# Kernel optimization log

Hardware: AMD Instinct MI355X
Metric: run time of the kernel (lower is better)

Reference implementation:

```python
import jax, jax.numpy as jnp
import numpy as np

N = 100000
E = 1280000
D = 64


def setup_inputs() -> dict:
    key = jax.random.key(0)
    k1, k2, k3, k4, k5, k6 = jax.random.split(key, 6)
    return {
        "x": jax.random.normal(k1, (N, D), dtype=jnp.float32),
        "w_src": jax.random.normal(k2, (D,), dtype=jnp.float32),
        "w_dst": jax.random.normal(k3, (D,), dtype=jnp.float32),
        "ew": jax.random.normal(k4, (E,), dtype=jnp.float32),
        "src_idx": jax.random.randint(k5, (E,), 0, N, dtype=jnp.int64),
        "dst_idx": jax.random.randint(k6, (E,), 0, N, dtype=jnp.int64),
    }


def reference(x, w_src, w_dst, ew, src_idx, dst_idx):
    # Per-node scalar scores: Linear(emb_dim, 1, bias=False)
    a_src = x @ w_src            # [N]
    a_dst = x @ w_dst            # [N]
    # Edge attention: tanh(a_src[u] + a_dst[v]) * ew  (u_add_v + tanh + scale)
    a = jnp.tanh(a_src[src_idx] + a_dst[dst_idx]) * ew   # [E]
    # Message = a_e * x[src_e]; reduce = scatter-sum over dst (u_mul_e + sum)
    m = a[:, None] * x[src_idx]                           # [E, D]
    h = jax.ops.segment_sum(m, dst_idx, num_segments=N)   # [N, D]
    return h
```

## Files before the change

kernel.cpp:

```cpp
#include <hip/hip_runtime.h>
#include <hip/hip_fp16.h>
#include <math.h>

typedef unsigned long long ull;

#define DIM  64
#define SPAN 256
#define SPAN_SHIFT 8
#define NBIN 256
#define KMAX 512
#define CAP  6144

__global__ __launch_bounds__(256) void score_hist_kernel(
        const float* __restrict__ x,
        const float* __restrict__ w_src,
        const float* __restrict__ w_dst,
        const int* __restrict__ dst_idx,
        float* __restrict__ a_src,
        float* __restrict__ a_dst,
        __half* __restrict__ xh,
        int* __restrict__ cnt,
        int N, int E, int K) {
    __shared__ int lh[KMAX];
    int tid = threadIdx.x;
    int b   = blockIdx.x;
    bool histblk = (b < NBIN);
    if (histblk) {
        for (int j = tid; j < K; j += 256) lh[j] = 0;
        __syncthreads();
    }
    int lane = tid & 63;
    int wave = tid >> 6;
    int grp  = lane >> 4;
    int sub  = lane & 15;
    int node = b * 16 + wave * 4 + grp;
    if (node < N) {
        float4 v  = ((const float4*)x)[(size_t)node * 16 + sub];
        float4 ws = ((const float4*)w_src)[sub];
        float4 wd = ((const float4*)w_dst)[sub];
        float s1 = v.x * ws.x + v.y * ws.y + v.z * ws.z + v.w * ws.w;
        float s2 = v.x * wd.x + v.y * wd.y + v.z * wd.z + v.w * wd.w;
        #pragma unroll
        for (int off = 1; off < 16; off <<= 1) {
            s1 += __shfl_xor(s1, off, 64);
            s2 += __shfl_xor(s2, off, 64);
        }
        if (sub == 0) { a_src[node] = s1; a_dst[node] = s2; }
        __half2 h01 = __floats2half2_rn(v.x, v.y);
        __half2 h23 = __floats2half2_rn(v.z, v.w);
        uint2 hv;
        hv.x = *(unsigned*)&h01;
        hv.y = *(unsigned*)&h23;
        *(uint2*)(xh + (size_t)node * DIM + (sub << 2)) = hv;
    }
    if (histblk) {
        for (int base = b * 2048; base < E; base += NBIN * 2048) {
            for (int off = tid << 1; off < 2048; off += 512) {
                int e = base + off;
                if (e + 1 < E) {
                    int2 t2 = *(const int2*)(dst_idx + e);
                    unsigned t0 = (unsigned)t2.x; if (t0 >= (unsigned)N) t0 = 0;
                    unsigned t1 = (unsigned)t2.y; if (t1 >= (unsigned)N) t1 = 0;
                    atomicAdd(&lh[t0 >> SPAN_SHIFT], 1);
                    atomicAdd(&lh[t1 >> SPAN_SHIFT], 1);
                } else if (e < E) {
                    unsigned t = (unsigned)dst_idx[e];
                    if (t >= (unsigned)N) t = 0;
                    atomicAdd(&lh[t >> SPAN_SHIFT], 1);
                }
            }
        }
        __syncthreads();
        for (int j = tid; j < K; j += 256) cnt[j * NBIN + b] = lh[j];
    }
}

__global__ void scan_part(const int* __restrict__ cnt, int* __restrict__ offs,
                          int* __restrict__ bsum, int N) {
    __shared__ int buf[2][256];
    int tid = threadIdx.x;
    int i = blockIdx.x * 256 + tid;
    int v = (i < N) ? cnt[i] : 0;
    int sel = 0;
    buf[0][tid] = v;
    __syncthreads();
    for (int off = 1; off < 256; off <<= 1) {
        int nsel = sel ^ 1;
        buf[nsel][tid] = buf[sel][tid] + ((tid >= off) ? buf[sel][tid - off] : 0);
        __syncthreads();
        sel = nsel;
    }
    if (i < N) offs[i] = buf[sel][tid] - v;
    if (tid == 255) bsum[blockIdx.x] = buf[sel][255];
}

__global__ __launch_bounds__(1024) void binpass_kernel(
        const float* __restrict__ ew,
        const int* __restrict__ src_idx,
        const int* __restrict__ dst_idx,
        const float* __restrict__ a_src,
        const float* __restrict__ a_dst,
        const int* __restrict__ moffs,
        const int* __restrict__ bsum,
        int* __restrict__ gbase,
        ull* __restrict__ pay,
        int E, int N, int K, int NBs) {
    __shared__ int lcur[KMAX];
    __shared__ int buf[2][512];
    int tid = threadIdx.x;
    int b   = blockIdx.x;
    int v = 0;
    if (tid < 512) {
        v = (tid < NBs) ? bsum[tid] : 0;
        buf[0][tid] = v;
    }
    __syncthreads();
    int sel = 0;
    for (int off = 1; off < 512; off <<= 1) {
        if (tid < 512)
            buf[sel ^ 1][tid] = buf[sel][tid] +
                                ((tid >= off) ? buf[sel][tid - off] : 0);
        __syncthreads();
        sel ^= 1;
    }
    int esel = sel ^ 1;
    if (tid < 512) buf[esel][tid] = buf[sel][tid] - v;
    __syncthreads();
    if (b == 0 && tid < 512) {
        if (tid < NBs) gbase[tid] = buf[esel][tid];
        if (tid == NBs) gbase[NBs] = E;
    }
    for (int j = tid; j < K; j += 1024)
        lcur[j] = moffs[j * NBIN + b] + buf[esel][j];
    __syncthreads();
    for (int base = b * 2048; base < E; base += NBIN * 2048) {
        int e = base + (tid << 1);
        if (e + 1 < E) {
            int2   s2 = *(const int2*)(src_idx + e);
            int2   t2 = *(const int2*)(dst_idx + e);
            float2 w2 = *(const float2*)(ew + e);
            unsigned s0 = (unsigned)s2.x; if (s0 >= (unsigned)N) s0 = 0;
            unsigned t0 = (unsigned)t2.x; if (t0 >= (unsigned)N) t0 = 0;
            unsigned s1 = (unsigned)s2.y; if (s1 >= (unsigned)N) s1 = 0;
            unsigned t1 = (unsigned)t2.y; if (t1 >= (unsigned)N) t1 = 0;
            float a0 = tanhf(a_src[s0] + a_dst[t0]) * w2.x;
            float a1 = tanhf(a_src[s1] + a_dst[t1]) * w2.y;
            int p0 = atomicAdd(&lcur[t0 >> SPAN_SHIFT], 1);
            int p1 = atomicAdd(&lcur[t1 >> SPAN_SHIFT], 1);
            unsigned r0 = (s0 << 8) | (t0 & (SPAN - 1u));
            unsigned r1 = (s1 << 8) | (t1 & (SPAN - 1u));
            pay[p0] = ((ull)r0 << 32) | (ull)__float_as_uint(a0);
            pay[p1] = ((ull)r1 << 32) | (ull)__float_as_uint(a1);
        } else if (e < E) {
            unsigned s = (unsigned)src_idx[e];
            unsigned t = (unsigned)dst_idx[e];
            if (s >= (unsigned)N) s = 0;
            if (t >= (unsigned)N) t = 0;
            float a = tanhf(a_src[s] + a_dst[t]) * ew[e];
            int pos = atomicAdd(&lcur[t >> SPAN_SHIFT], 1);
            unsigned rec = (s << 8) | (t & (SPAN - 1u));
            pay[pos] = ((ull)rec << 32) | (ull)__float_as_uint(a);
        }
    }
}

__global__ __launch_bounds__(1024) void sort_gather_kernel(
        const __half* __restrict__ xh,
        const float* __restrict__ x32,
        const ull* __restrict__ pay,
        const int* __restrict__ gbase,
        float* __restrict__ h,
        int N, int K, int E) {
    __shared__ ull srec[CAP];
    __shared__ unsigned short sidx[CAP];
    __shared__ int hcnt[SPAN];
    __shared__ int hoff[2][SPAN];
    __shared__ int lcur[SPAN];
    __shared__ int nstart[SPAN];
    int tid = threadIdx.x;
    int b   = blockIdx.x;
    int bstart = gbase[b];
    int bend   = gbase[b + 1];
    int cnt = bend - bstart;

    if (cnt <= CAP) {
        if (tid < SPAN) hcnt[tid] = 0;
        __syncthreads();
        for (int i = tid; i < cnt; i += 1024) {
            ull r = pay[bstart + i];
            srec[i] = r;
            atomicAdd(&hcnt[(int)((r >> 32) & (SPAN - 1u))], 1);
        }
        __syncthreads();
        int sel = 0;
        if (tid < SPAN) hoff[0][tid] = hcnt[tid];
        __syncthreads();
        for (int off = 1; off < SPAN; off <<= 1) {
            int nsel = sel ^ 1;
            if (tid < SPAN)
                hoff[nsel][tid] = hoff[sel][tid] +
                                  ((tid >= off) ? hoff[sel][tid - off] : 0);
            __syncthreads();
            sel = nsel;
        }
        if (tid < SPAN) {
            int excl = hoff[sel][tid] - hcnt[tid];
            nstart[tid] = excl;
            lcur[tid]   = excl;
        }
        __syncthreads();
        for (int i = tid; i < cnt; i += 1024) {
            ull r = srec[i];
            int d = (int)((r >> 32) & (SPAN - 1u));
            int pos = atomicAdd(&lcur[d], 1);
            sidx[pos] = (unsigned short)i;
        }
        __syncthreads();
        int lane = tid & 63;
        int wave = tid >> 6;
        int grp  = lane >> 4;
        int sub  = lane & 15;
        for (int d = wave; d < SPAN; d += 16) {
            int node = b * SPAN + d;
            if (node >= N) break;
            int p  = nstart[d];
            int pe = p + hcnt[d];
            float ax = 0.f, ay = 0.f, az = 0.f, aw = 0.f;
            while (p + 8 <= pe) {
                ull r0 = srec[sidx[p + grp]];
                ull r1 = srec[sidx[p + 4 + grp]];
                p += 8;
                unsigned s0 = (unsigned)(r0 >> 40); if (s0 >= (unsigned)N) s0 = 0;
                unsigned s1 = (unsigned)(r1 >> 40); if (s1 >= (unsigned)N) s1 = 0;
                uint2 v0 = *(const uint2*)(xh + (size_t)s0 * DIM + (sub << 2));
                uint2 v1 = *(const uint2*)(xh + (size_t)s1 * DIM + (sub << 2));
                float a0 = __uint_as_float((unsigned)r0);
                float a1 = __uint_as_float((unsigned)r1);
                float2 l0 = __half22float2(*(const __half2*)&v0.x);
                float2 h0 = __half22float2(*(const __half2*)&v0.y);
                float2 l1 = __half22float2(*(const __half2*)&v1.x);
                float2 h1 = __half22float2(*(const __half2*)&v1.y);
                ax = fmaf(a0, l0.x, ax); ay = fmaf(a0, l0.y, ay);
                az = fmaf(a0, h0.x, az); aw = fmaf(a0, h0.y, aw);
                ax = fmaf(a1, l1.x, ax); ay = fmaf(a1, l1.y, ay);
                az = fmaf(a1, h1.x, az); aw = fmaf(a1, h1.y, aw);
            }
            while (p < pe) {
                int q = p + grp;
                float a0 = 0.f;
                unsigned s0 = 0;
                if (q < pe) {
                    ull r0 = srec[sidx[q]];
                    a0 = __uint_as_float((unsigned)r0);
                    s0 = (unsigned)(r0 >> 40); if (s0 >= (unsigned)N) s0 = 0;
                }
                p += 4;
                uint2 v0 = *(const uint2*)(xh + (size_t)s0 * DIM + (sub << 2));
                float2 l0 = __half22float2(*(const __half2*)&v0.x);
                float2 h0 = __half22float2(*(const __half2*)&v0.y);
                ax = fmaf(a0, l0.x, ax); ay = fmaf(a0, l0.y, ay);
                az = fmaf(a0, h0.x, az); aw = fmaf(a0, h0.y, aw);
            }
            ax += __shfl_xor(ax, 16, 64); ay += __shfl_xor(ay, 16, 64);
            az += __shfl_xor(az, 16, 64); aw += __shfl_xor(aw, 16, 64);
            ax += __shfl_xor(ax, 32, 64); ay += __shfl_xor(ay, 32, 64);
            az += __shfl_xor(az, 32, 64); aw += __shfl_xor(aw, 32, 64);
            if (grp == 0) {
                float4 out = make_float4(ax, ay, az, aw);
                *(float4*)(h + (size_t)node * DIM + (sub << 2)) = out;
            }
        }
    } else {
        for (int j = tid; j < SPAN * DIM; j += 1024) {
            int node = b * SPAN + (j >> 6);
            if (node < N) h[(size_t)node * DIM + (j & 63)] = 0.f;
        }
        __syncthreads();
        for (int i = tid; i < cnt; i += 1024) {
            ull r = pay[bstart + i];
            unsigned s = (unsigned)(r >> 40);
            if (s >= (unsigned)N) s = 0;
            int node = b * SPAN + (int)((r >> 32) & (SPAN - 1u));
            float a = __uint_as_float((unsigned)r);
            if (node < N)
                for (int k = 0; k < DIM; ++k)
                    atomicAdd(&h[(size_t)node * DIM + k],
                              a * x32[(size_t)s * DIM + k]);
        }
    }
}

__global__ void zero_h_kernel(float* __restrict__ p, int n) {
    int i = blockIdx.x * blockDim.x + threadIdx.x;
    if (i < n) p[i] = 0.f;
}

__global__ void edge_kernel_atomic(const float* __restrict__ x,
                                   const float* __restrict__ ew,
                                   const int* __restrict__ src_idx,
                                   const int* __restrict__ dst_idx,
                                   const float* __restrict__ a_src,
                                   const float* __restrict__ a_dst,
                                   float* __restrict__ h,
                                   int E) {
    int gid  = blockIdx.x * blockDim.x + threadIdx.x;
    int e    = gid >> 6;
    int lane = threadIdx.x & 63;
    if (e >= E) return;
    int s = src_idx[e];
    int t = dst_idx[e];
    float a  = tanhf(a_src[s] + a_dst[t]) * ew[e];
    float xv = x[(size_t)s * DIM + lane];
    atomicAdd(&h[(size_t)t * DIM + lane], a * xv);
}

__global__ void score_only_kernel(const float* __restrict__ x,
                                  const float* __restrict__ w_src,
                                  const float* __restrict__ w_dst,
                                  float* __restrict__ a_src,
                                  float* __restrict__ a_dst,
                                  int N) {
    int gid  = blockIdx.x * blockDim.x + threadIdx.x;
    int node = gid >> 6;
    int lane = threadIdx.x & 63;
    if (node >= N) return;
    float xv = x[(size_t)node * DIM + lane];
    float s1 = xv * w_src[lane];
    float s2 = xv * w_dst[lane];
    #pragma unroll
    for (int off = 32; off > 0; off >>= 1) {
        s1 += __shfl_down(s1, off, 64);
        s2 += __shfl_down(s2, off, 64);
    }
    if (lane == 0) {
        a_src[node] = s1;
        a_dst[node] = s2;
    }
}

extern "C" void kernel_launch(void* const* d_in, const int* in_sizes, int n_in,
                              void* d_out, int out_size, void* d_ws, size_t ws_size,
                              hipStream_t stream) {
    const float* x     = (const float*)d_in[0];
    const float* w_src = (const float*)d_in[1];
    const float* w_dst = (const float*)d_in[2];
    const float* ew    = (const float*)d_in[3];
    const int*   src   = (const int*)d_in[4];
    const int*   dst   = (const int*)d_in[5];
    float* h = (float*)d_out;

    int N = in_sizes[0] / DIM;
    int E = in_sizes[3];

    int K    = (N + SPAN - 1) / SPAN;
    int Ntot = K * NBIN;
    int NBs  = (Ntot + 255) / 256;
    int sh_blocks = (N + 15) / 16;

    float* a_src  = (float*)d_ws;
    float* a_dst  = a_src + N;
    int*   moffs  = (int*)(a_dst + N);
    int*   bsum   = moffs + Ntot + 1;
    int*   gbase  = bsum + NBs;
    size_t head_bytes = ((size_t)(2 * N) + (size_t)Ntot + 1 + (size_t)NBs +
                         (size_t)(K + 1)) * 4;
    size_t pay_off = (head_bytes + 15) & ~(size_t)15;
    ull* pay = (ull*)((char*)d_ws + pay_off);
    size_t xh_off = pay_off + (size_t)E * 8;
    __half* xh = (__half*)((char*)d_ws + xh_off);
    size_t need = xh_off + (size_t)N * DIM * 2;

    if (ws_size < need || K > KMAX || K < 1 || NBs != K || NBs > 512 ||
        sh_blocks < NBIN || (N * DIM) % 2 != 0) {
        int score_blocks = (N + 3) / 4;
        score_only_kernel<<<score_blocks, 256, 0, stream>>>(x, w_src, w_dst,
                                                            a_src, a_dst, N);
        int ob = (out_size + 255) / 256;
        zero_h_kernel<<<ob, 256, 0, stream>>>(h, out_size);
        int edge_blocks = (E + 3) / 4;
        edge_kernel_atomic<<<edge_blocks, 256, 0, stream>>>(x, ew, src, dst,
                                                            a_src, a_dst, h, E);
        return;
    }

    score_hist_kernel<<<sh_blocks, 256, 0, stream>>>(x, w_src, w_dst, dst,
                                                     a_src, a_dst, xh, moffs,
                                                     N, E, K);
    scan_part<<<NBs, 256, 0, stream>>>(moffs, moffs, bsum, Ntot);
    binpass_kernel<<<NBIN, 1024, 0, stream>>>(ew, src, dst, a_src, a_dst,
                                              moffs, bsum, gbase, pay,
                                              E, N, K, NBs);
    sort_gather_kernel<<<K, 1024, 0, stream>>>(xh, x, pay, gbase,
                                               h, N, K, E);
}
```

Before: 166.0 us.

## Fold scan kernel into binpass by recomputing per-bin prefix sums per block

Removes the separate scan_part launch. Each binpass block now reads the raw count matrix and computes its own per-bucket totals and per-block exclusive prefixes with wave reductions, then does the bucket-level scan in shared memory. This saves one kernel launch and its global round-trip, but every block redundantly reads the full count matrix. CAP is also lowered from 6144 to 4096, which affects the sort_gather kernel's capacity or shared-memory use. That could change occupancy or force more overflow handling.

Result: slower. 178.2 us (+7.3%).

```diff
diff --git a/kernel.cpp b/kernel.cpp
--- a/kernel.cpp
+++ b/kernel.cpp
@@ -9,7 +9,7 @@
 #define SPAN_SHIFT 8
 #define NBIN 256
 #define KMAX 512
-#define CAP  6144
+#define CAP  4096
 
 __global__ __launch_bounds__(256) void score_hist_kernel(
         const float* __restrict__ x,
@@ -75,63 +75,53 @@
     }
 }
 
-__global__ void scan_part(const int* __restrict__ cnt, int* __restrict__ offs,
-                          int* __restrict__ bsum, int N) {
-    __shared__ int buf[2][256];
-    int tid = threadIdx.x;
-    int i = blockIdx.x * 256 + tid;
-    int v = (i < N) ? cnt[i] : 0;
-    int sel = 0;
-    buf[0][tid] = v;
-    __syncthreads();
-    for (int off = 1; off < 256; off <<= 1) {
-        int nsel = sel ^ 1;
-        buf[nsel][tid] = buf[sel][tid] + ((tid >= off) ? buf[sel][tid - off] : 0);
-        __syncthreads();
-        sel = nsel;
-    }
-    if (i < N) offs[i] = buf[sel][tid] - v;
-    if (tid == 255) bsum[blockIdx.x] = buf[sel][255];
-}
-
 __global__ __launch_bounds__(1024) void binpass_kernel(
         const float* __restrict__ ew,
         const int* __restrict__ src_idx,
         const int* __restrict__ dst_idx,
         const float* __restrict__ a_src,
         const float* __restrict__ a_dst,
-        const int* __restrict__ moffs,
-        const int* __restrict__ bsum,
+        const int* __restrict__ cnt,
         int* __restrict__ gbase,
         ull* __restrict__ pay,
-        int E, int N, int K, int NBs) {
+        int E, int N, int K) {
     __shared__ int lcur[KMAX];
-    __shared__ int buf[2][512];
-    int tid = threadIdx.x;
-    int b   = blockIdx.x;
-    int v = 0;
-    if (tid < 512) {
-        v = (tid < NBs) ? bsum[tid] : 0;
-        buf[0][tid] = v;
+    __shared__ int rows[KMAX];
+    __shared__ int sbuf[2][512];
+    int tid  = threadIdx.x;
+    int b    = blockIdx.x;
+    int lane = tid & 63;
+    int wave = tid >> 6;
+    for (int j = wave; j < K; j += 16) {
+        int4 c4 = ((const int4*)(cnt + j * NBIN))[lane];
+        int i0 = lane << 2;
+        int tot = c4.x + c4.y + c4.z + c4.w;
+        int par = ((i0 + 0) < b ? c4.x : 0) + ((i0 + 1) < b ? c4.y : 0) +
+                  ((i0 + 2) < b ? c4.z : 0) + ((i0 + 3) < b ? c4.w : 0);
+        #pragma unroll
+        for (int off = 32; off > 0; off >>= 1) {
+            tot += __shfl_down(tot, off, 64);
+            par += __shfl_down(par, off, 64);
+        }
+        if (lane == 0) { rows[j] = tot; lcur[j] = par; }
     }
     __syncthreads();
     int sel = 0;
+    if (tid < 512) sbuf[0][tid] = (tid < K) ? rows[tid] : 0;
+    __syncthreads();
     for (int off = 1; off < 512; off <<= 1) {
         if (tid < 512)
-            buf[sel ^ 1][tid] = buf[sel][tid] +
-                                ((tid >= off) ? buf[sel][tid - off] : 0);
+            sbuf[sel ^ 1][tid] = sbuf[sel][tid] +
+                                 ((tid >= off) ? sbuf[sel][tid - off] : 0);
         __syncthreads();
         sel ^= 1;
     }
-    int esel = sel ^ 1;
-    if (tid < 512) buf[esel][tid] = buf[sel][tid] - v;
-    __syncthreads();
-    if (b == 0 && tid < 512) {
-        if (tid < NBs) gbase[tid] = buf[esel][tid];
-        if (tid == NBs) gbase[NBs] = E;
-    }
-    for (int j = tid; j < K; j += 1024)
-        lcur[j] = moffs[j * NBIN + b] + buf[esel][j];
+    if (tid < K) {
+        int gex = sbuf[sel][tid] - rows[tid];
+        lcur[tid] += gex;
+        if (b == 0) gbase[tid] = gex;
+    }
+    if (b == 0 && tid == 0) gbase[K] = E;
     __syncthreads();
     for (int base = b * 2048; base < E; base += NBIN * 2048) {
         int e = base + (tid << 1);
@@ -354,24 +344,21 @@
 
     int K    = (N + SPAN - 1) / SPAN;
     int Ntot = K * NBIN;
-    int NBs  = (Ntot + 255) / 256;
     int sh_blocks = (N + 15) / 16;
 
     float* a_src  = (float*)d_ws;
     float* a_dst  = a_src + N;
-    int*   moffs  = (int*)(a_dst + N);
-    int*   bsum   = moffs + Ntot + 1;
-    int*   gbase  = bsum + NBs;
-    size_t head_bytes = ((size_t)(2 * N) + (size_t)Ntot + 1 + (size_t)NBs +
-                         (size_t)(K + 1)) * 4;
+    int*   cnt    = (int*)(a_dst + N);
+    int*   gbase  = cnt + Ntot;
+    size_t head_bytes = ((size_t)(2 * N) + (size_t)Ntot + (size_t)(K + 1)) * 4;
     size_t pay_off = (head_bytes + 15) & ~(size_t)15;
     ull* pay = (ull*)((char*)d_ws + pay_off);
     size_t xh_off = pay_off + (size_t)E * 8;
     __half* xh = (__half*)((char*)d_ws + xh_off);
     size_t need = xh_off + (size_t)N * DIM * 2;
 
-    if (ws_size < need || K > KMAX || K < 1 || NBs != K || NBs > 512 ||
-        sh_blocks < NBIN || (N * DIM) % 2 != 0) {
+    if (ws_size < need || K > KMAX || K < 1 || sh_blocks < NBIN ||
+        (N * DIM) % 2 != 0) {
         int score_blocks = (N + 3) / 4;
         score_only_kernel<<<score_blocks, 256, 0, stream>>>(x, w_src, w_dst,
                                                             a_src, a_dst, N);
@@ -384,12 +371,10 @@
     }
 
     score_hist_kernel<<<sh_blocks, 256, 0, stream>>>(x, w_src, w_dst, dst,
-                                                     a_src, a_dst, xh, moffs,
+                                                     a_src, a_dst, xh, cnt,
                                                      N, E, K);
-    scan_part<<<NBs, 256, 0, stream>>>(moffs, moffs, bsum, Ntot);
     binpass_kernel<<<NBIN, 1024, 0, stream>>>(ew, src, dst, a_src, a_dst,
-                                              moffs, bsum, gbase, pay,
-                                              E, N, K, NBs);
+                                              cnt, gbase, pay, E, N, K);
     sort_gather_kernel<<<K, 1024, 0, stream>>>(xh, x, pay, gbase,
                                                h, N, K, E);
 }
```
